# Kernel optimization log

Hardware: AMD Instinct MI355X
Metric: run time of the kernel (lower is better)

Reference implementation:

```python
import jax, jax.numpy as jnp
import numpy as np

N_P, N_D, N_S = 100000, 1000, 5000      # patients, drugs, diseases
C, H, L = 64, 4, 2                       # hidden, heads, layers
DH = C // H                              # head dim
IN_P, IN_D, IN_S = 64, 128, 64           # raw feature dims per node type
E_PD, E_DP, E_DS, E_PS = 300000, 300000, 100000, 100000
EPS = 1e-16


def setup_inputs() -> dict:
    key = jax.random.key(0)
    ks = jax.random.split(key, 20)

    def lin(k, fin, fout, prefix=()):
        return jax.random.normal(k, prefix + (fin, fout), jnp.float32) / np.sqrt(fin).astype(np.float32)

    def edges(k, e, n_src, n_dst):
        k1, k2 = jax.random.split(k)
        return jnp.stack([jax.random.randint(k1, (e,), 0, n_src),
                          jax.random.randint(k2, (e,), 0, n_dst)]).astype(jnp.int32)

    inp = {}
    inp['x_p'] = jax.random.normal(ks[0], (N_P, IN_P), jnp.float32)
    inp['x_d'] = jax.random.normal(ks[1], (N_D, IN_D), jnp.float32)
    inp['x_s'] = jax.random.normal(ks[2], (N_S, IN_S), jnp.float32)
    inp['Win_p'] = lin(ks[3], IN_P, C); inp['bin_p'] = jnp.zeros((C,), jnp.float32)
    inp['Win_d'] = lin(ks[4], IN_D, C); inp['bin_d'] = jnp.zeros((C,), jnp.float32)
    inp['Win_s'] = lin(ks[5], IN_S, C); inp['bin_s'] = jnp.zeros((C,), jnp.float32)
    inp['Wk'] = lin(ks[6], C, C, (L, 3)); inp['bk'] = jnp.zeros((L, 3, C), jnp.float32)
    inp['Wq'] = lin(ks[7], C, C, (L, 3)); inp['bq'] = jnp.zeros((L, 3, C), jnp.float32)
    inp['Wv'] = lin(ks[8], C, C, (L, 3)); inp['bv'] = jnp.zeros((L, 3, C), jnp.float32)
    inp['Wa'] = lin(ks[9], C, C, (L, 3)); inp['ba'] = jnp.zeros((L, 3, C), jnp.float32)
    inp['a_rel'] = jax.random.normal(ks[10], (L, 4, H, DH, DH), jnp.float32) / np.sqrt(DH).astype(np.float32)
    inp['m_rel'] = jax.random.normal(ks[11], (L, 4, H, DH, DH), jnp.float32) / np.sqrt(DH).astype(np.float32)
    inp['p_rel'] = jnp.ones((L, 4, H), jnp.float32)   # PyG inits rel prior to ones
    inp['skip'] = jnp.ones((L, 3), jnp.float32)       # PyG inits skip gate to ones
    inp['ei_pd'] = edges(ks[12], E_PD, N_P, N_D)  # patient -takes-> drug
    inp['ei_dp'] = edges(ks[13], E_DP, N_D, N_P)  # drug -taken_by-> patient
    inp['ei_ds'] = edges(ks[14], E_DS, N_D, N_S)  # drug -treats-> disease
    inp['ei_ps'] = edges(ks[15], E_PS, N_P, N_S)  # patient -has-> disease
    return inp


def _hgt(x_p, x_d, x_s, Win_p, bin_p, Win_d, bin_d, Win_s, bin_s,
         Wk, bk, Wq, bq, Wv, bv, Wa, ba, a_rel, m_rel, p_rel, skip,
         ei_pd, ei_dp, ei_ds, ei_ps):
    Ns = (N_P, N_D, N_S)
    # per-node-type input projection (lin_dict)
    xs = [x_p @ Win_p + bin_p, x_d @ Win_d + bin_d, x_s @ Win_s + bin_s]
    # (src_type, dst_type, edge_index) for each relation
    edge_defs = [(0, 1, ei_pd), (1, 0, ei_dp), (1, 2, ei_ds), (0, 2, ei_ps)]
    inv_sqrt_d = np.float32(1.0 / np.sqrt(DH))

    for l in range(L):  # HGTConv layers
        k_t = [(xs[t] @ Wk[l, t] + bk[l, t]).reshape(Ns[t], H, DH) for t in range(3)]
        q_t = [(xs[t] @ Wq[l, t] + bq[l, t]).reshape(Ns[t], H, DH) for t in range(3)]
        v_t = [(xs[t] @ Wv[l, t] + bv[l, t]).reshape(Ns[t], H, DH) for t in range(3)]
        out = [jnp.zeros((Ns[t], H, DH), xs[t].dtype) for t in range(3)]
        for r, (st, dt, ei) in enumerate(edge_defs):
            src, dst = ei[0], ei[1]
            # relation-specific head-wise transforms of K and V
            k_rel = jnp.einsum('nhd,hde->nhe', k_t[st], a_rel[l, r])
            v_rel = jnp.einsum('nhd,hde->nhe', v_t[st], m_rel[l, r])
            # attention logits per edge, per head: [E, H]
            alpha = (q_t[dt][dst] * k_rel[src]).sum(-1) * (p_rel[l, r] * inv_sqrt_d)
            # segment softmax over incoming edges of each dst node (per relation)
            mx = jax.ops.segment_max(alpha, dst, num_segments=Ns[dt])
            a = jnp.exp(alpha - jax.lax.stop_gradient(mx)[dst])
            den = jax.ops.segment_sum(a, dst, num_segments=Ns[dt])
            a = a / (den[dst] + EPS)
            # attention-weighted scatter-add of messages, grouped by 'sum'
            out[dt] = out[dt] + jax.ops.segment_sum(v_rel[src] * a[:, :, None], dst, num_segments=Ns[dt])
        new_xs = []
        for t in range(3):
            o = jax.nn.gelu(out[t].reshape(Ns[t], C), approximate=False) @ Wa[l, t] + ba[l, t]
            s = jax.nn.sigmoid(skip[l, t])  # learned skip gate (in == out channels)
            new_xs.append(s * o + (1.0 - s) * xs[t])
        xs = new_xs
    # concatenate node-type outputs along node axis: [N_P+N_D+N_S, C]
    return jnp.concatenate(xs, axis=0)


def reference(x_p, x_d, x_s, Win_p, bin_p, Win_d, bin_d, Win_s, bin_s,
              Wk, bk, Wq, bq, Wv, bv, Wa, ba, a_rel, m_rel, p_rel, skip,
              ei_pd, ei_dp, ei_ds, ei_ps):
    return _hgt(x_p, x_d, x_s, Win_p, bin_p, Win_d, bin_d, Win_s, bin_s,
                Wk, bk, Wq, bq, Wv, bv, Wa, ba, a_rel, m_rel, p_rel, skip,
                ei_pd, ei_dp, ei_ds, ei_ps)
```

## Files before the change

kernel.cpp:

```cpp
#include <hip/hip_runtime.h>
#include <cmath>

typedef unsigned short ush;
typedef __attribute__((ext_vector_type(8))) short short8;
typedef __attribute__((ext_vector_type(4))) float floatx4;

static constexpr int N_P = 100000, N_D = 1000, N_S = 5000, NT = N_P + N_D + N_S;
static constexpr int NC = 111000;
static constexpr int E_TOT = 800000;

static constexpr int NB0 = 128, NB2 = 64, NB3 = 64;
static constexpr int CH0 = (300000 + NB0 - 1) / NB0;
static constexpr int CH2 = (100000 + NB2 - 1) / NB2;
static constexpr int HB0_OFF = 0;
static constexpr int HB2_OFF = NB0 * 1000;
static constexpr int HB3_OFF = HB2_OFF + NB2 * 5000;
static constexpr int NCH0 = NB0 / 16, NCH2 = NB2 / 16;
static constexpr int CS0_OFF = 0;
static constexpr int CS2_OFF = NCH0 * 1000;
static constexpr int CS3_OFF = CS2_OFF + NCH2 * 5000;
static constexpr int NHIST = NB0 + NB2 + NB3;
static constexpr int NBLK_R1 = (300000 + 255) / 256;
static constexpr int NZB = (100000 + 255) / 256;

__device__ __forceinline__ float b2f(ush b) { return __uint_as_float(((unsigned)b) << 16); }
__device__ __forceinline__ ush f2b(float f) {
    unsigned u = __float_as_uint(f);
    return (ush)((u + 0x7FFFu + ((u >> 16) & 1u)) >> 16);
}

static constexpr size_t OFF_WINP = 0;
static constexpr size_t OFF_BINP = 4096;
static constexpr size_t OFF_WIND = 4160;
static constexpr size_t OFF_BIND = 12352;
static constexpr size_t OFF_WINS = 12416;
static constexpr size_t OFF_BINS = 16512;
static constexpr size_t OFF_WK = 16576;
static constexpr size_t OFF_BK = 41152;
static constexpr size_t OFF_WQ = 41536;
static constexpr size_t OFF_BQ = 66112;
static constexpr size_t OFF_WV = 66496;
static constexpr size_t OFF_BV = 91072;
static constexpr size_t OFF_WA = 91456;
static constexpr size_t OFF_BA = 116032;
static constexpr size_t OFF_AREL = 116416;
static constexpr size_t OFF_MREL = 124608;
static constexpr size_t OFF_PREL = 132800;
static constexpr size_t OFF_SKIP = 132832;
static constexpr size_t CW_TOTAL = 132838;
static constexpr int NCONVB = (int)((CW_TOTAL + 255) / 256);
static constexpr int NSCB = (NC + 1 + 255) / 256;

static constexpr size_t TWINP = 0;
static constexpr size_t TWIND = 4096;
static constexpr size_t TWINS = 12288;
static constexpr size_t TWQO = 16384;
static constexpr size_t TWAO = 40960;
static constexpr size_t TW_TOTAL = 65536;
static constexpr int NTWB = (int)(TW_TOTAL / 256);

struct ConvArgs {
    const void* src[18];
    long cum[19];
    int fl[18];
};

struct CsrB {
    const int* ei[3];
    const int* ei1;
};

__device__ __forceinline__ void hist_geom(int b, const CsrB& c, int& r, const int*& ei, int& E,
                                          int& ndst, int& e0, int& e1, int& hb) {
    if (b < NB0) {
        r = 0; ei = c.ei[0]; E = 300000; ndst = 1000;
        e0 = b * CH0; hb = HB0_OFF + b * 1000;
    } else if (b < NB0 + NB2) {
        r = 1; ei = c.ei[1]; E = 100000; ndst = 5000;
        e0 = (b - NB0) * CH2; hb = HB2_OFF + (b - NB0) * 5000;
    } else {
        r = 2; ei = c.ei[2]; E = 100000; ndst = 5000;
        e0 = (b - NB0 - NB2) * CH2; hb = HB3_OFF + (b - NB0 - NB2) * 5000;
    }
    e1 = min(E, e0 + ((r == 0) ? CH0 : CH2));
}

__device__ __forceinline__ bool cs_geom(int g, int& idx0, int& step) {
    if (g >= 48000) return false;
    if (g < 8000) {
        int c = g / 1000, d = g % 1000;
        idx0 = HB0_OFF + c * 16 * 1000 + d; step = 1000;
    } else if (g < 28000) {
        int gg = g - 8000, c = gg / 5000, d = gg % 5000;
        idx0 = HB2_OFF + c * 16 * 5000 + d; step = 5000;
    } else {
        int gg = g - 28000, c = gg / 5000, d = gg % 5000;
        idx0 = HB3_OFF + c * 16 * 5000 + d; step = 5000;
    }
    return true;
}

__global__ __launch_bounds__(256) void k1_kernel(ConvArgs a, ush* __restrict__ dst,
                                                 ush* __restrict__ tw,
                                                 int* __restrict__ cnt_r1, CsrB c,
                                                 int* __restrict__ HB) {
    const int b = blockIdx.x;
    if (b < NCONVB) {
        long g = (long)b * 256 + threadIdx.x;
        if (g >= (long)CW_TOTAL) return;
        int t = 0;
        while (g >= a.cum[t + 1]) t++;
        long i = g - a.cum[t];
        float v = a.fl[t] ? ((const float*)a.src[t])[i] : b2f(((const ush*)a.src[t])[i]);
        dst[g] = f2b(v);
    } else if (b < NCONVB + NZB) {
        int g = (b - NCONVB) * 256 + threadIdx.x;
        if (g < 100000) cnt_r1[g] = 0;
    } else if (b < NCONVB + NZB + NHIST) {
        __shared__ int h[5000];
        int r, E, ndst, e0, e1, hb;
        const int* ei;
        hist_geom(b - NCONVB - NZB, c, r, ei, E, ndst, e0, e1, hb);
        for (int d = threadIdx.x; d < ndst; d += 256) h[d] = 0;
        __syncthreads();
        for (int e = e0 + threadIdx.x; e < e1; e += 256) atomicAdd(&h[ei[E + e]], 1);
        __syncthreads();
        for (int d = threadIdx.x; d < ndst; d += 256) HB[hb + d] = h[d];
    } else {
        int g = (b - NCONVB - NZB - NHIST) * 256 + threadIdx.x;
        const void* src; int fl; long ibase; int e;
        if (g < 4096) { src = a.src[0]; fl = a.fl[0]; e = g; ibase = 0; }
        else if (g < 12288) { src = a.src[2]; fl = a.fl[2]; e = g - 4096; ibase = 0; }
        else if (g < 16384) { src = a.src[4]; fl = a.fl[4]; e = g - 12288; ibase = 0; }
        else if (g < 40960) { int ee = g - 16384; src = a.src[8]; fl = a.fl[8];
                              e = ee & 4095; ibase = (long)(ee >> 12) * 4096; }
        else { int ee = g - 40960; src = a.src[12]; fl = a.fl[12];
               e = ee & 4095; ibase = (long)(ee >> 12) * 4096; }
        int f = e >> 9, l = (e >> 3) & 63, j = e & 7;
        int s = f >> 2, cc = f & 3;
        long in = ibase + (long)(32 * s + ((l >> 4) << 3) + j) * 64 + 16 * cc + (l & 15);
        float v = fl ? ((const float*)src)[in] : b2f(((const ush*)src)[in]);
        tw[g] = f2b(v);
    }
}

template <int K>
__device__ __forceinline__ void stage_A(short* sA, const ush* __restrict__ X, int M, int row0) {
    for (int cid = threadIdx.x; cid < 64 * K / 8; cid += 256) {
        int r = cid / (K / 8), c0 = (cid % (K / 8)) * 8;
        int row = row0 + r;
        short8 v = {0, 0, 0, 0, 0, 0, 0, 0};
        if (row < M) v = *(const short8*)(const void*)(X + (size_t)row * K + c0);
        *(short8*)(&sA[r * (K + 8) + c0]) = v;
    }
}

template <int K>
__device__ __forceinline__ void stage_A_raw(short* sA, const void* __restrict__ X, int f,
                                            int M, int row0) {
    for (int cid = threadIdx.x; cid < 64 * K / 8; cid += 256) {
        int r = cid / (K / 8), c0 = (cid % (K / 8)) * 8;
        int row = row0 + r;
        short8 v = {0, 0, 0, 0, 0, 0, 0, 0};
        if (row < M) {
            if (f) {
                const floatx4* fp = (const floatx4*)((const float*)X + (size_t)row * K + c0);
                floatx4 f0 = fp[0], f1 = fp[1];
#pragma unroll
                for (int j = 0; j < 4; j++) v[j] = (short)f2b(f0[j]);
#pragma unroll
                for (int j = 0; j < 4; j++) v[4 + j] = (short)f2b(f1[j]);
            } else {
                v = *(const short8*)(const void*)((const ush*)X + (size_t)row * K + c0);
            }
        }
        *(short8*)(&sA[r * (K + 8) + c0]) = v;
    }
}

template <int K>
__device__ __forceinline__ void gemm_core64(const short* sA, short* sB,
                                            const ush* __restrict__ W, const ush* __restrict__ Bb,
                                            ush* __restrict__ Y, int M, int row0) {
    constexpr int NF = (K / 32) * 4;
    const int tid = threadIdx.x;
    for (int u = tid; u < NF * 64; u += 256)
        *(short8*)(&sB[u * 8]) = *(const short8*)(const void*)(W + (size_t)u * 8);
    __syncthreads();
    const int w = tid >> 6, l = tid & 63;
    floatx4 acc[4];
#pragma unroll
    for (int c = 0; c < 4; c++) {
        float bv = b2f(Bb[16 * c + (l & 15)]);
        acc[c] = (floatx4){bv, bv, bv, bv};
    }
#pragma unroll
    for (int s = 0; s < K / 32; s++) {
        short8 a = *(const short8*)(&sA[(16 * w + (l & 15)) * (K + 8) + 32 * s + ((l >> 4) << 3)]);
#pragma unroll
        for (int c = 0; c < 4; c++) {
            short8 b = *(const short8*)(&sB[(s * 4 + c) * 512 + l * 8]);
            acc[c] = __builtin_amdgcn_mfma_f32_16x16x32_bf16(a, b, acc[c], 0, 0, 0);
        }
    }
    __syncthreads();
#pragma unroll
    for (int c = 0; c < 4; c++)
#pragma unroll
        for (int r = 0; r < 4; r++)
            sB[(16 * w + ((l >> 4) << 2) + r) * 72 + 16 * c + (l & 15)] =
                (short)f2b(acc[c][r]);
    __syncthreads();
    for (int u = tid; u < 512; u += 256) {
        int r = u >> 3, c0 = (u & 7) * 8;
        int row = row0 + r;
        if (row < M)
            *(short8*)(Y + (size_t)row * 64 + c0) = *(const short8*)(&sB[r * 72 + c0]);
    }
}

template <int NG>
__device__ __forceinline__ void gemm_wide(const short* sA, short* sB,
                                          const ush* __restrict__ Wq, const ush* __restrict__ Bq,
                                          ush* __restrict__ Yq,
                                          const ush* __restrict__ WeA,
                                          ush* __restrict__ YAk, ush* __restrict__ YAv,
                                          const ush* __restrict__ WeB,
                                          ush* __restrict__ YBk, ush* __restrict__ YBv,
                                          int M, int row0) {
    constexpr int NF = 2 * NG;
    const int tid = threadIdx.x;
    for (int u = tid; u < NF * 64; u += 256) {
        int f = u >> 6, k = u & 63;
        int s = f / NG, c = f % NG;
        const ush* src;
        if (c < 4) src = Wq + (size_t)(s * 4 + c) * 512;
        else if (c < 12) src = WeA + (size_t)(s * 8 + (c - 4)) * 512;
        else src = WeB + (size_t)(s * 8 + (c - 12)) * 512;
        *(short8*)(&sB[f * 512 + k * 8]) = *(const short8*)(const void*)(src + k * 8);
    }
    __syncthreads();
    const int w = tid >> 6, l = tid & 63;
    floatx4 acc[NG];
#pragma unroll
    for (int c = 0; c < NG; c++) {
        float bv;
        if (c < 4) bv = b2f(Bq[16 * c + (l & 15)]);
        else if (c < 12) bv = b2f(WeA[8192 + 16 * (c - 4) + (l & 15)]);
        else bv = b2f(WeB[8192 + 16 * (c - 12) + (l & 15)]);
        acc[c] = (floatx4){bv, bv, bv, bv};
    }
#pragma unroll
    for (int s = 0; s < 2; s++) {
        short8 a = *(const short8*)(&sA[(16 * w + (l & 15)) * 72 + 32 * s + ((l >> 4) << 3)]);
#pragma unroll
        for (int c = 0; c < NG; c++) {
            short8 b = *(const short8*)(&sB[(s * NG + c) * 512 + l * 8]);
            acc[c] = __builtin_amdgcn_mfma_f32_16x16x32_bf16(a, b, acc[c], 0, 0, 0);
        }
    }
    ush* dst[5] = {Yq, YAk, YAv, YBk, YBv};
#pragma unroll
    for (int cg = 0; cg < NG / 4; cg++) {
        __syncthreads();
#pragma unroll
        for (int c2 = 0; c2 < 4; c2++)
#pragma unroll
            for (int r = 0; r < 4; r++)
                sB[(16 * w + ((l >> 4) << 2) + r) * 72 + 16 * c2 + (l & 15)] =
                    (short)f2b(acc[cg * 4 + c2][r]);
        __syncthreads();
        ush* Y = dst[cg];
        for (int u = tid; u < 512; u += 256) {
            int r = u >> 3, c0 = (u & 7) * 8;
            int row = row0 + r;
            if (row < M)
                *(short8*)(Y + (size_t)row * 64 + c0) = *(const short8*)(&sB[r * 72 + c0]);
        }
    }
}

struct K2Args {
    const void* raw[3];
    int f[3];
    const ush* W[3];
    const ush* Bb[3];
    ush* X;
    const int* HB;
    int* CS;
    int* cnt;
    const int* ei1;
};

__global__ __launch_bounds__(256) void k2_kernel(K2Args a) {
    extern __shared__ short smem[];
    const int b = blockIdx.x;
    if (b < 1658) {
        if (b < 1563) {
            short* sA = smem; short* sB = smem + 64 * 72;
            stage_A_raw<64>(sA, a.raw[0], a.f[0], N_P, b * 64);
            gemm_core64<64>(sA, sB, a.W[0], a.Bb[0], a.X, N_P, b * 64);
        } else if (b < 1579) {
            short* sA = smem; short* sB = smem + 64 * 136;
            stage_A_raw<128>(sA, a.raw[1], a.f[1], N_D, (b - 1563) * 64);
            gemm_core64<128>(sA, sB, a.W[1], a.Bb[1], a.X + (size_t)N_P * 64, N_D,
                             (b - 1563) * 64);
        } else {
            short* sA = smem; short* sB = smem + 64 * 72;
            stage_A_raw<64>(sA, a.raw[2], a.f[2], N_S, (b - 1579) * 64);
            gemm_core64<64>(sA, sB, a.W[2], a.Bb[2], a.X + (size_t)(N_P + N_D) * 64, N_S,
                            (b - 1579) * 64);
        }
    } else if (b < 1701) {
        int d = (b - 1658) * 256 + threadIdx.x;
        if (d >= 11000) return;
        int ld_, nch, base, step, cs0, csstep, roff;
        if (d < 1000) { ld_ = d; nch = NCH0; base = HB0_OFF + ld_; step = 1000;
                        cs0 = CS0_OFF + ld_; csstep = 1000; roff = 0; }
        else if (d < 6000) { ld_ = d - 1000; nch = NCH2; base = HB2_OFF + ld_; step = 5000;
                             cs0 = CS2_OFF + ld_; csstep = 5000; roff = 101000; }
        else { ld_ = d - 6000; nch = NCH2; base = HB3_OFF + ld_; step = 5000;
               cs0 = CS3_OFF + ld_; csstep = 5000; roff = 106000; }
        int run = 0;
        for (int cc = 0; cc < nch; cc++) {
            int s = 0;
#pragma unroll
            for (int bb = 0; bb < 16; bb++) s += a.HB[base + (cc * 16 + bb) * step];
            a.CS[cs0 + cc * csstep] = run;
            run += s;
        }
        a.cnt[roff + ld_] = run;
    } else {
        int g = (b - 1701) * 256 + threadIdx.x;
        if (g < 300000) atomicAdd(&a.cnt[1000 + a.ei1[300000 + g]], 1);
    }
}

__global__ __launch_bounds__(256) void k3_kernel(const int* __restrict__ cnt,
                                                 int* __restrict__ tmp,
                                                 int* __restrict__ part,
                                                 const ush* __restrict__ CW,
                                                 ush* __restrict__ weff) {
    const int b = blockIdx.x;
    if (b < 109) {
        __shared__ int ls[256];
        const int t = threadIdx.x;
        const int base = b * 1024 + t * 4;
        int v[4];
#pragma unroll
        for (int j = 0; j < 4; j++) v[j] = (base + j < NC) ? cnt[base + j] : 0;
        int tsum = v[0] + v[1] + v[2] + v[3];
        ls[t] = tsum;
        __syncthreads();
        for (int off = 1; off < 256; off <<= 1) {
            int y = (t >= off) ? ls[t - off] : 0;
            __syncthreads();
            ls[t] += y;
            __syncthreads();
        }
        int run = ls[t] - tsum;
#pragma unroll
        for (int j = 0; j < 4; j++) {
            if (base + j < NC) tmp[base + j] = run;
            run += v[j];
        }
        if (t == 255) part[b] = ls[255];
    } else {
        const int eb = b - 109;
        const int l = eb >> 2, r = eb & 3;
        const int st_of[4] = {0, 1, 1, 0};
        const int st = st_of[r];
        ush* out = weff + (size_t)eb * 8320;
        for (int idx = threadIdx.x; idx < 8320; idx += 256) {
            int k, n;
            if (idx < 8192) {
                int f = idx >> 9, ll = (idx >> 3) & 63, j = idx & 7;
                int s = f >> 3, c = f & 7;
                k = 32 * s + ((ll >> 4) << 3) + j;
                n = 16 * c + (ll & 15);
            } else { k = -1; n = idx - 8192; }
            int kv = n >= 64;
            int jj = n & 63, h = jj >> 4, e = jj & 15;
            const ush* W = CW + (kv ? OFF_WV : OFF_WK) + (size_t)(l * 3 + st) * 4096;
            const ush* B = CW + (kv ? OFF_BV : OFF_BK) + (size_t)(l * 3 + st) * 64;
            const ush* R = CW + (kv ? OFF_MREL : OFF_AREL) + (size_t)(l * 4 + r) * 1024;
            float acc = 0.f;
            if (k >= 0) {
#pragma unroll
                for (int d = 0; d < 16; d++)
                    acc += b2f(W[k * 64 + h * 16 + d]) * b2f(R[h * 256 + d * 16 + e]);
            } else {
#pragma unroll
                for (int d = 0; d < 16; d++)
                    acc += b2f(B[h * 16 + d]) * b2f(R[h * 256 + d * 16 + e]);
            }
            out[idx] = f2b(acc);
        }
    }
}

__global__ __launch_bounds__(256) void k4_kernel(const int* __restrict__ tmp,
                                                 const int* __restrict__ part,
                                                 int* __restrict__ rowptr,
                                                 int* __restrict__ HB,
                                                 const int* __restrict__ CS,
                                                 int* __restrict__ fillpos) {
    const int b = blockIdx.x;
    if (b < NSCB) {
        __shared__ int ls[256];
        const int t = threadIdx.x;
        ls[t] = (t < 109) ? part[t] : 0;
        __syncthreads();
        for (int off = 1; off < 256; off <<= 1) {
            int y = (t >= off) ? ls[t - off] : 0;
            __syncthreads();
            ls[t] += y;
            __syncthreads();
        }
        int i = b * 256 + t;
        if (i <= NC)
            rowptr[i] = (i == NC) ? ls[255] : tmp[i] + ((i >> 10) ? ls[(i >> 10) - 1] : 0);
    } else if (b < NSCB + 188) {
        int g = (b - NSCB) * 256 + threadIdx.x;
        int idx0, step;
        if (!cs_geom(g, idx0, step)) return;
        int run = CS[g];
#pragma unroll
        for (int bb = 0; bb < 16; bb++) {
            int t2 = HB[idx0 + bb * step];
            HB[idx0 + bb * step] = run;
            run += t2;
        }
    } else {
        int g = (b - NSCB - 188) * 256 + threadIdx.x;
        if (g < 100000) fillpos[g] = 0;
    }
}

struct QKVArgs {
    const ush* X;
    ush* Q;
    ush* KVk[4];
    ush* KVv[4];
    const ush* Wq[3];
    const ush* Bq[3];
    const ush* We[4];
};

__global__ __launch_bounds__(256) void qkv_kernel(QKVArgs a) {
    extern __shared__ short smem[];
    const int b = blockIdx.x;
    short* sA = smem;
    short* sB = smem + 64 * 72;
    if (b < 1563) {
        stage_A<64>(sA, a.X, N_P, b * 64);
        gemm_wide<20>(sA, sB, a.Wq[0], a.Bq[0], a.Q,
                      a.We[0], a.KVk[0], a.KVv[0],
                      a.We[3], a.KVk[3], a.KVv[3], N_P, b * 64);
    } else if (b < 1579) {
        int lb = b - 1563;
        stage_A<64>(sA, a.X + (size_t)N_P * 64, N_D, lb * 64);
        gemm_wide<20>(sA, sB, a.Wq[1], a.Bq[1], a.Q + (size_t)N_P * 64,
                      a.We[1], a.KVk[1], a.KVv[1],
                      a.We[2], a.KVk[2], a.KVv[2], N_D, lb * 64);
    } else {
        int lb = b - 1579;
        stage_A<64>(sA, a.X + (size_t)(N_P + N_D) * 64, N_S, lb * 64);
        gemm_wide<4>(sA, sB, a.Wq[2], a.Bq[2], a.Q + (size_t)(N_P + N_D) * 64,
                     nullptr, nullptr, nullptr, nullptr, nullptr, nullptr,
                     N_S, lb * 64);
    }
}

struct FillArgs {
    CsrB cb;
    const int* HB;
    const int* rowptr;
    int* fillpos;
    int* col;
};

__global__ __launch_bounds__(256) void fill_kernel(FillArgs a) {
    extern __shared__ short smem[];
    const int b = blockIdx.x;
    if (b < NHIST) {
        int* h = (int*)smem;
        int r, E, ndst, e0, e1, hb;
        const int* ei;
        hist_geom(b, a.cb, r, ei, E, ndst, e0, e1, hb);
        const int roff = (r == 0) ? 0 : (r == 1) ? 101000 : 106000;
        for (int d = threadIdx.x; d < ndst; d += 256) h[d] = a.rowptr[roff + d] + a.HB[hb + d];
        __syncthreads();
        for (int e = e0 + threadIdx.x; e < e1; e += 256) {
            int d = ei[E + e];
            int slot = atomicAdd(&h[d], 1);
            a.col[slot] = ei[e];
        }
    } else {
        int g = (b - NHIST) * 256 + threadIdx.x;
        if (g < 300000) {
            int gi = 1000 + a.cb.ei1[300000 + g];
            int slot = a.rowptr[gi] + atomicAdd(&a.fillpos[gi], 1);
            a.col[slot] = a.cb.ei1[g];
        }
    }
}

struct AggrArgs {
    const int* rowptr;
    const int* col;
    const ush* KVk[4];
    const ush* KVv[4];
    const ush* Q;
    const ush* prel;
    ush* OUT;
};

template <int LANES>
__device__ __forceinline__ void seg_attn(const AggrArgs& a, int rel, int g, int h, int lane,
                                         const float* qf, float* o) {
    const int s0 = a.rowptr[g], s1 = a.rowptr[g + 1];
    const ush* Kb = a.KVk[rel];
    const ush* Vb = a.KVv[rel];
    const float ps = b2f(a.prel[rel * 4 + h]) * 0.25f;
    float m = -1e30f, s = 0.f;
    float acc[16];
#pragma unroll
    for (int i = 0; i < 16; i++) acc[i] = 0.f;
    int j = s0 + lane;
    if (j < s1) {
        {
            int src = a.col[j];
            const ush* kp = Kb + (size_t)src * 64 + h * 16;
            const ush* vp = Vb + (size_t)src * 64 + h * 16;
            short8 k0 = *(const short8*)(const void*)kp;
            short8 k1 = *(const short8*)(const void*)(kp + 8);
            short8 v0 = *(const short8*)(const void*)vp;
            short8 v1 = *(const short8*)(const void*)(vp + 8);
            float dot = 0.f;
#pragma unroll
            for (int i = 0; i < 8; i++) dot += qf[i] * b2f((ush)k0[i]);
#pragma unroll
            for (int i = 0; i < 8; i++) dot += qf[8 + i] * b2f((ush)k1[i]);
            m = dot * ps;
            s = 1.f;
#pragma unroll
            for (int i = 0; i < 8; i++) acc[i] = b2f((ush)v0[i]);
#pragma unroll
            for (int i = 0; i < 8; i++) acc[8 + i] = b2f((ush)v1[i]);
        }
        for (j += LANES; j < s1; j += LANES) {
            int src = a.col[j];
            const ush* kp = Kb + (size_t)src * 64 + h * 16;
            const ush* vp = Vb + (size_t)src * 64 + h * 16;
            short8 k0 = *(const short8*)(const void*)kp;
            short8 k1 = *(const short8*)(const void*)(kp + 8);
            short8 v0 = *(const short8*)(const void*)vp;
            short8 v1 = *(const short8*)(const void*)(vp + 8);
            float dot = 0.f;
#pragma unroll
            for (int i = 0; i < 8; i++) dot += qf[i] * b2f((ush)k0[i]);
#pragma unroll
            for (int i = 0; i < 8; i++) dot += qf[8 + i] * b2f((ush)k1[i]);
            float e1 = __expf(dot * ps - m);
            s += e1;
#pragma unroll
            for (int i = 0; i < 8; i++) acc[i] += e1 * b2f((ush)v0[i]);
#pragma unroll
            for (int i = 0; i < 8; i++) acc[8 + i] += e1 * b2f((ush)v1[i]);
        }
    }
#pragma unroll
    for (int wd = LANES >> 1; wd >= 1; wd >>= 1) {
        float mo = __shfl_xor(m, wd);
        float so = __shfl_xor(s, wd);
        float nm = fmaxf(m, mo);
        float e0 = __expf(m - nm), e1 = __expf(mo - nm);
        s = s * e0 + so * e1;
#pragma unroll
        for (int i = 0; i < 16; i++) {
            float ao = __shfl_xor(acc[i], wd);
            acc[i] = acc[i] * e0 + ao * e1;
        }
        m = nm;
    }
    float inv = 1.f / (s + 1e-16f);
#pragma unroll
    for (int i = 0; i < 16; i++) o[i] += acc[i] * inv;
}

template <int LANES>
__device__ __forceinline__ void job_run(const AggrArgs& a, int wid, int nd, int rel, int roff,
                                        size_t xoff, int rel2, int roff2) {
    const int lane = wid % LANES;
    const int grp = wid / LANES;
    const int d = grp >> 2, h = grp & 3;
    if (d >= nd) return;
    const ush* qp = a.Q + xoff + (size_t)d * 64 + h * 16;
    short8 q0 = *(const short8*)(const void*)qp;
    short8 q1 = *(const short8*)(const void*)(qp + 8);
    float qf[16];
#pragma unroll
    for (int i = 0; i < 8; i++) { qf[i] = b2f((ush)q0[i]); qf[8 + i] = b2f((ush)q1[i]); }
    float o[16];
#pragma unroll
    for (int i = 0; i < 16; i++) o[i] = 0.f;
    seg_attn<LANES>(a, rel, roff + d, h, lane, qf, o);
    if (rel2 >= 0) seg_attn<LANES>(a, rel2, roff2 + d, h, lane, qf, o);
    if (lane == 0) {
        ush* op = a.OUT + xoff + (size_t)d * 64 + h * 16;
        short8 w0, w1;
#pragma unroll
        for (int i = 0; i < 8; i++) {
            float va = o[i];
            w0[i] = (short)f2b(0.5f * va * (1.0f + erff(va * 0.70710678118654752f)));
            float vb = o[8 + i];
            w1[i] = (short)f2b(0.5f * vb * (1.0f + erff(vb * 0.70710678118654752f)));
        }
        *(short8*)(op) = w0;
        *(short8*)(op + 8) = w1;
    }
}

__global__ __launch_bounds__(256) void aggr_kernel(AggrArgs a) {
    const int b = blockIdx.x, t = threadIdx.x;
    if (b < 250) {
        job_run<16>(a, b * 256 + t, N_D, 0, 0, (size_t)N_P * 64, -1, 0);
    } else if (b < 563) {
        job_run<4>(a, (b - 250) * 256 + t, N_S, 2, 101000, (size_t)(N_P + N_D) * 64, 3, 106000);
    } else {
        job_run<2>(a, (b - 563) * 256 + t, N_P, 1, 1000, 0, -1, 0);
    }
}

struct EpiArgs {
    const ush* O;
    ush* X;
    const ush* W[3];
    const ush* Bb[3];
    const ush* skipv;
    void* fout;
    int foutf;
    int last;
};

__global__ __launch_bounds__(256) void epi_kernel(EpiArgs a) {
    const int b = blockIdx.x;
    int t, lb, M;
    size_t noff;
    if (b < 1563) { t = 0; lb = b; M = N_P; noff = 0; }
    else if (b < 1579) { t = 1; lb = b - 1563; M = N_D; noff = (size_t)N_P; }
    else { t = 2; lb = b - 1579; M = N_S; noff = (size_t)(N_P + N_D); }
    const ush* O = a.O + noff * 64;
    ush* X = a.X + noff * 64;
    const ush* WF = a.W[t];
    __shared__ short sA[64 * 72];
    __shared__ short sB[8 * 512];
    const int tid = threadIdx.x;
    const int row0 = lb * 64;
    for (int cid = tid; cid < 512; cid += 256) {
        int r = cid >> 3, c0 = (cid & 7) * 8;
        int row = row0 + r;
        short8 sv = {0, 0, 0, 0, 0, 0, 0, 0};
        if (row < M) sv = *(const short8*)(const void*)(O + (size_t)row * 64 + c0);
        *(short8*)(&sA[r * 72 + c0]) = sv;
    }
    for (int u = tid; u < 512; u += 256)
        *(short8*)(&sB[u * 8]) = *(const short8*)(const void*)(WF + (size_t)u * 8);
    __syncthreads();
    const float sg = 1.f / (1.f + expf(-b2f(a.skipv[t])));
    const int w = tid >> 6, l = tid & 63;
    floatx4 acc[4];
#pragma unroll
    for (int c = 0; c < 4; c++) {
        float bv = b2f(a.Bb[t][16 * c + (l & 15)]);
        acc[c] = (floatx4){bv, bv, bv, bv};
    }
#pragma unroll
    for (int s = 0; s < 2; s++) {
        short8 av = *(const short8*)(&sA[(16 * w + (l & 15)) * 72 + 32 * s + ((l >> 4) << 3)]);
#pragma unroll
        for (int c = 0; c < 4; c++) {
            short8 bv = *(const short8*)(&sB[(s * 4 + c) * 512 + l * 8]);
            acc[c] = __builtin_amdgcn_mfma_f32_16x16x32_bf16(av, bv, acc[c], 0, 0, 0);
        }
    }
    float* sOf = (float*)sA;
#pragma unroll
    for (int ch = 0; ch < 2; ch++) {
        __syncthreads();
        if ((w >> 1) == ch) {
#pragma unroll
            for (int c = 0; c < 4; c++)
#pragma unroll
                for (int r = 0; r < 4; r++)
                    sOf[(16 * (w & 1) + ((l >> 4) << 2) + r) * 68 + 16 * c + (l & 15)] =
                        acc[c][r];
        }
        __syncthreads();
        {
            int r = tid >> 3, c0 = (tid & 7) * 8;
            int row = row0 + ch * 32 + r;
            if (row < M) {
                floatx4 f0 = *(const floatx4*)(&sOf[r * 68 + c0]);
                floatx4 f1 = *(const floatx4*)(&sOf[r * 68 + c0 + 4]);
                short8 xv = *(const short8*)(const void*)(X + (size_t)row * 64 + c0);
                float vo[8];
#pragma unroll
                for (int j = 0; j < 4; j++) vo[j] = sg * f0[j] + (1.f - sg) * b2f((ush)xv[j]);
#pragma unroll
                for (int j = 0; j < 4; j++)
                    vo[4 + j] = sg * f1[j] + (1.f - sg) * b2f((ush)xv[4 + j]);
                if (!a.last) {
                    short8 ov;
#pragma unroll
                    for (int j = 0; j < 8; j++) ov[j] = (short)f2b(vo[j]);
                    *(short8*)(X + (size_t)row * 64 + c0) = ov;
                } else {
                    size_t goff = (noff + row) * 64 + c0;
                    if (a.foutf) {
                        floatx4 o0, o1;
#pragma unroll
                        for (int j = 0; j < 4; j++) { o0[j] = vo[j]; o1[j] = vo[4 + j]; }
                        *(floatx4*)((float*)a.fout + goff) = o0;
                        *(floatx4*)((float*)a.fout + goff + 4) = o1;
                    } else {
                        short8 ov;
#pragma unroll
                        for (int j = 0; j < 8; j++) ov[j] = (short)f2b(vo[j]);
                        *(short8*)((ush*)a.fout + goff) = ov;
                    }
                }
            }
        }
    }
}

extern "C" void kernel_launch(void* const* d_in, const int* in_sizes, int n_in,
                              void* d_out, int out_size, void* d_ws, size_t ws_size,
                              hipStream_t stream) {
    char* w = (char*)d_ws;
    w += 64;
    ush* CW = (ush*)w;      w += ((CW_TOTAL * 2 + 63) / 64) * 64;
    ush* WEFFB = (ush*)w;   w += ((size_t)8 * 8320 * 2 + 63) / 64 * 64;
    ush* TW = (ush*)w;      w += (size_t)TW_TOTAL * 2;
    ush* X = (ush*)w;       w += (size_t)NT * 64 * 2;
    ush* Q = (ush*)w;       w += (size_t)NT * 64 * 2;
    ush* KV0 = (ush*)w;     w += (size_t)N_P * 128 * 2;
    ush* KV1 = (ush*)w;     w += (size_t)N_D * 128 * 2;
    ush* KV2 = (ush*)w;     w += (size_t)N_D * 128 * 2;
    ush* KV3 = (ush*)w;     w += (size_t)N_P * 128 * 2;
    ush* OUT = (ush*)w;     w += (size_t)NT * 64 * 4;
    int* CNT = (int*)w;     w += (size_t)NC * 4;
    int* TMP = (int*)w;     w += (size_t)NC * 4;
    int* PART = (int*)w;    w += 512;
    int* ROWPTR = (int*)w;  w += (size_t)(NC + 1) * 4;
    int* COL = (int*)w;     w += (size_t)E_TOT * 4;
    int* HB = (int*)OUT;
    int* CS = (int*)OUT + 800000;

    static const long sz[18] = {4096, 64, 8192, 64, 4096, 64, 24576, 384, 24576, 384,
                                24576, 384, 24576, 384, 8192, 8192, 32, 6};
    ConvArgs ca;
    long cum = 0;
    for (int t = 0; t < 18; t++) {
        ca.src[t] = d_in[3 + t];
        ca.cum[t] = cum;
        ca.fl[t] = (in_sizes[3 + t] != (int)(sz[t] * 2)) ? 1 : 0;
        cum += sz[t];
    }
    ca.cum[18] = cum;

    CsrB cb;
    cb.ei[0] = (const int*)d_in[21];
    cb.ei[1] = (const int*)d_in[23];
    cb.ei[2] = (const int*)d_in[24];
    cb.ei1 = (const int*)d_in[22];

    k1_kernel<<<NCONVB + NZB + NHIST + NTWB, 256, 0, stream>>>(ca, CW, TW, CNT + 1000, cb, HB);

    K2Args k2;
    k2.raw[0] = d_in[0]; k2.f[0] = (in_sizes[0] != N_P * 64 * 2) ? 1 : 0;
    k2.raw[1] = d_in[1]; k2.f[1] = (in_sizes[1] != N_D * 128 * 2) ? 1 : 0;
    k2.raw[2] = d_in[2]; k2.f[2] = (in_sizes[2] != N_S * 64 * 2) ? 1 : 0;
    k2.W[0] = TW + TWINP; k2.Bb[0] = CW + OFF_BINP;
    k2.W[1] = TW + TWIND; k2.Bb[1] = CW + OFF_BIND;
    k2.W[2] = TW + TWINS; k2.Bb[2] = CW + OFF_BINS;
    k2.X = X;
    k2.HB = HB; k2.CS = CS; k2.cnt = CNT; k2.ei1 = cb.ei1;
    k2_kernel<<<1701 + NBLK_R1, 256, 33792, stream>>>(k2);

    k3_kernel<<<109 + 8, 256, 0, stream>>>(CNT, TMP, PART, CW, WEFFB);

    k4_kernel<<<NSCB + 188 + NZB, 256, 0, stream>>>(TMP, PART, ROWPTR, HB, CS, CNT + 1000);

    ush* KVr[4] = {KV0, KV1, KV2, KV3};
    const size_t nsr[4] = {(size_t)N_P, (size_t)N_D, (size_t)N_D, (size_t)N_P};
    const int foutf = (out_size != NT * 64 * 2) ? 1 : 0;

    for (int l = 0; l < 2; l++) {
        QKVArgs qk;
        qk.X = X;
        qk.Q = Q;
        for (int r = 0; r < 4; r++) {
            qk.KVk[r] = KVr[r];
            qk.KVv[r] = KVr[r] + nsr[r] * 64;
            qk.We[r] = WEFFB + (size_t)(l * 4 + r) * 8320;
        }
        for (int t = 0; t < 3; t++) {
            qk.Wq[t] = TW + TWQO + (size_t)(l * 3 + t) * 4096;
            qk.Bq[t] = CW + OFF_BQ + (l * 3 + t) * 64;
        }
        qkv_kernel<<<1658, 256, 50176, stream>>>(qk);

        if (l == 0) {
            FillArgs fa;
            fa.cb = cb;
            fa.HB = HB;
            fa.rowptr = ROWPTR;
            fa.fillpos = CNT;
            fa.col = COL;
            fill_kernel<<<NHIST + NBLK_R1, 256, 20000, stream>>>(fa);
        }

        AggrArgs aa;
        aa.rowptr = ROWPTR;
        aa.col = COL;
        for (int r = 0; r < 4; r++) {
            aa.KVk[r] = KVr[r];
            aa.KVv[r] = KVr[r] + nsr[r] * 64;
        }
        aa.Q = Q;
        aa.prel = CW + OFF_PREL + l * 16;
        aa.OUT = OUT;
        aggr_kernel<<<3688, 256, 0, stream>>>(aa);

        EpiArgs ea;
        ea.O = OUT;
        ea.X = X;
        for (int t = 0; t < 3; t++) {
            ea.W[t] = TW + TWAO + (size_t)(l * 3 + t) * 4096;
            ea.Bb[t] = CW + OFF_BA + (l * 3 + t) * 64;
        }
        ea.skipv = CW + OFF_SKIP + l * 3;
        ea.fout = d_out;
        ea.foutf = foutf;
        ea.last = (l == 1) ? 1 : 0;
        epi_kernel<<<1658, 256, 0, stream>>>(ea);
    }
}
```

Baseline: 386.0 us.

## Process QKV GEMM in 64-column panels and widen aggregation lanes for hubs

The fused Q/K/V projection now loads weights and runs MFMAs one 64-column output panel at a time, reusing a small shared buffer, instead of staging all 20 column groups at once. This cuts dynamic shared memory from about 50 KB to about 17 KB and drops the 20-accumulator register array, aiming at higher occupancy, in exchange for more barriers and repeated weight staging. Separately, the aggregation kernel gives more lanes per destination node for the high-degree drug and disease segments, launching more blocks to spread their long edge lists.

```diff
diff --git a/kernel.cpp b/kernel.cpp
--- a/kernel.cpp
+++ b/kernel.cpp
@@ -219,63 +219,62 @@
     }
 }
 
-template <int NG>
-__device__ __forceinline__ void gemm_wide(const short* sA, short* sB,
-                                          const ush* __restrict__ Wq, const ush* __restrict__ Bq,
-                                          ush* __restrict__ Yq,
-                                          const ush* __restrict__ WeA,
-                                          ush* __restrict__ YAk, ush* __restrict__ YAv,
-                                          const ush* __restrict__ WeB,
-                                          ush* __restrict__ YBk, ush* __restrict__ YBv,
-                                          int M, int row0) {
-    constexpr int NF = 2 * NG;
+template <int NP>
+__device__ __forceinline__ void gemm_panels(short* sA, short* sB,
+                                            const ush* __restrict__ Wq,
+                                            const ush* __restrict__ Bq, ush* __restrict__ Yq,
+                                            const ush* __restrict__ WeA,
+                                            ush* __restrict__ YAk, ush* __restrict__ YAv,
+                                            const ush* __restrict__ WeB,
+                                            ush* __restrict__ YBk, ush* __restrict__ YBv,
+                                            int M, int row0) {
     const int tid = threadIdx.x;
-    for (int u = tid; u < NF * 64; u += 256) {
-        int f = u >> 6, k = u & 63;
-        int s = f / NG, c = f % NG;
-        const ush* src;
-        if (c < 4) src = Wq + (size_t)(s * 4 + c) * 512;
-        else if (c < 12) src = WeA + (size_t)(s * 8 + (c - 4)) * 512;
-        else src = WeB + (size_t)(s * 8 + (c - 12)) * 512;
-        *(short8*)(&sB[f * 512 + k * 8]) = *(const short8*)(const void*)(src + k * 8);
-    }
+    const int w = tid >> 6, l = tid & 63;
     __syncthreads();
-    const int w = tid >> 6, l = tid & 63;
-    floatx4 acc[NG];
-#pragma unroll
-    for (int c = 0; c < NG; c++) {
-        float bv;
-        if (c < 4) bv = b2f(Bq[16 * c + (l & 15)]);
-        else if (c < 12) bv = b2f(WeA[8192 + 16 * (c - 4) + (l & 15)]);
-        else bv = b2f(WeB[8192 + 16 * (c - 12) + (l & 15)]);
-        acc[c] = (floatx4){bv, bv, bv, bv};
-    }
-#pragma unroll
-    for (int s = 0; s < 2; s++) {
-        short8 a = *(const short8*)(&sA[(16 * w + (l & 15)) * 72 + 32 * s + ((l >> 4) << 3)]);
-#pragma unroll
-        for (int c = 0; c < NG; c++) {
-            short8 b = *(const short8*)(&sB[(s * NG + c) * 512 + l * 8]);
-            acc[c] = __builtin_amdgcn_mfma_f32_16x16x32_bf16(a, b, acc[c], 0, 0, 0);
-        }
-    }
+    short8 a0 = *(const short8*)(&sA[(16 * w + (l & 15)) * 72 + ((l >> 4) << 3)]);
+    short8 a1 = *(const short8*)(&sA[(16 * w + (l & 15)) * 72 + 32 + ((l >> 4) << 3)]);
     ush* dst[5] = {Yq, YAk, YAv, YBk, YBv};
 #pragma unroll
-    for (int cg = 0; cg < NG / 4; cg++) {
-        __syncthreads();
-#pragma unroll
-        for (int c2 = 0; c2 < 4; c2++)
+    for (int p = 0; p < NP; p++) {
+        __syncthreads();
+        const ush* base = (p == 0) ? Wq : ((p <= 2) ? WeA : WeB);
+        const int nw = (p == 0) ? 4 : 8;
+        const int moff = (p == 0 || p == 1 || p == 3) ? 0 : 4;
+        for (int u = tid; u < 512; u += 256) {
+            int f = u >> 6, k = u & 63;
+            int s = f >> 2, c = f & 3;
+            const ush* src = base + (size_t)(s * nw + moff + c) * 512;
+            *(short8*)(&sB[f * 512 + k * 8]) = *(const short8*)(const void*)(src + k * 8);
+        }
+        __syncthreads();
+        const ush* bias = (p == 0) ? Bq : ((p <= 2) ? WeA + 8192 : WeB + 8192);
+        const int boff = (p == 0 || p == 1 || p == 3) ? 0 : 64;
+        floatx4 acc[4];
+#pragma unroll
+        for (int c = 0; c < 4; c++) {
+            float bv = b2f(bias[boff + 16 * c + (l & 15)]);
+            acc[c] = (floatx4){bv, bv, bv, bv};
+        }
+#pragma unroll
+        for (int c = 0; c < 4; c++) {
+            short8 b0 = *(const short8*)(&sB[c * 512 + l * 8]);
+            acc[c] = __builtin_amdgcn_mfma_f32_16x16x32_bf16(a0, b0, acc[c], 0, 0, 0);
+            short8 b1 = *(const short8*)(&sB[(4 + c) * 512 + l * 8]);
+            acc[c] = __builtin_amdgcn_mfma_f32_16x16x32_bf16(a1, b1, acc[c], 0, 0, 0);
+        }
+#pragma unroll
+        for (int c = 0; c < 4; c++)
 #pragma unroll
             for (int r = 0; r < 4; r++)
-                sB[(16 * w + ((l >> 4) << 2) + r) * 72 + 16 * c2 + (l & 15)] =
-                    (short)f2b(acc[cg * 4 + c2][r]);
-        __syncthreads();
-        ush* Y = dst[cg];
+                sA[(16 * w + ((l >> 4) << 2) + r) * 72 + 16 * c + (l & 15)] =
+                    (short)f2b(acc[c][r]);
+        __syncthreads();
+        ush* Y = dst[p];
         for (int u = tid; u < 512; u += 256) {
             int r = u >> 3, c0 = (u & 7) * 8;
             int row = row0 + r;
             if (row < M)
-                *(short8*)(Y + (size_t)row * 64 + c0) = *(const short8*)(&sB[r * 72 + c0]);
+                *(short8*)(Y + (size_t)row * 64 + c0) = *(const short8*)(&sA[r * 72 + c0]);
         }
     }
 }
@@ -454,21 +453,21 @@
     short* sB = smem + 64 * 72;
     if (b < 1563) {
         stage_A<64>(sA, a.X, N_P, b * 64);
-        gemm_wide<20>(sA, sB, a.Wq[0], a.Bq[0], a.Q,
-                      a.We[0], a.KVk[0], a.KVv[0],
-                      a.We[3], a.KVk[3], a.KVv[3], N_P, b * 64);
+        gemm_panels<5>(sA, sB, a.Wq[0], a.Bq[0], a.Q,
+                       a.We[0], a.KVk[0], a.KVv[0],
+                       a.We[3], a.KVk[3], a.KVv[3], N_P, b * 64);
     } else if (b < 1579) {
         int lb = b - 1563;
         stage_A<64>(sA, a.X + (size_t)N_P * 64, N_D, lb * 64);
-        gemm_wide<20>(sA, sB, a.Wq[1], a.Bq[1], a.Q + (size_t)N_P * 64,
-                      a.We[1], a.KVk[1], a.KVv[1],
-                      a.We[2], a.KVk[2], a.KVv[2], N_D, lb * 64);
+        gemm_panels<5>(sA, sB, a.Wq[1], a.Bq[1], a.Q + (size_t)N_P * 64,
+                       a.We[1], a.KVk[1], a.KVv[1],
+                       a.We[2], a.KVk[2], a.KVv[2], N_D, lb * 64);
     } else {
         int lb = b - 1579;
         stage_A<64>(sA, a.X + (size_t)(N_P + N_D) * 64, N_S, lb * 64);
-        gemm_wide<4>(sA, sB, a.Wq[2], a.Bq[2], a.Q + (size_t)(N_P + N_D) * 64,
-                     nullptr, nullptr, nullptr, nullptr, nullptr, nullptr,
-                     N_S, lb * 64);
+        gemm_panels<1>(sA, sB, a.Wq[2], a.Bq[2], a.Q + (size_t)(N_P + N_D) * 64,
+                       nullptr, nullptr, nullptr, nullptr, nullptr, nullptr,
+                       N_S, lb * 64);
     }
 }
 
@@ -624,12 +623,12 @@
 
 __global__ __launch_bounds__(256) void aggr_kernel(AggrArgs a) {
     const int b = blockIdx.x, t = threadIdx.x;
-    if (b < 250) {
-        job_run<16>(a, b * 256 + t, N_D, 0, 0, (size_t)N_P * 64, -1, 0);
-    } else if (b < 563) {
-        job_run<4>(a, (b - 250) * 256 + t, N_S, 2, 101000, (size_t)(N_P + N_D) * 64, 3, 106000);
+    if (b < 1000) {
+        job_run<64>(a, b * 256 + t, N_D, 0, 0, (size_t)N_P * 64, -1, 0);
+    } else if (b < 2250) {
+        job_run<16>(a, (b - 1000) * 256 + t, N_S, 2, 101000, (size_t)(N_P + N_D) * 64, 3, 106000);
     } else {
-        job_run<2>(a, (b - 563) * 256 + t, N_P, 1, 1000, 0, -1, 0);
+        job_run<2>(a, (b - 2250) * 256 + t, N_P, 1, 1000, 0, -1, 0);
     }
 }
 
@@ -811,7 +810,7 @@
             qk.Wq[t] = TW + TWQO + (size_t)(l * 3 + t) * 4096;
             qk.Bq[t] = CW + OFF_BQ + (l * 3 + t) * 64;
         }
-        qkv_kernel<<<1658, 256, 50176, stream>>>(qk);
+        qkv_kernel<<<1658, 256, 17408, stream>>>(qk);
 
         if (l == 0) {
             FillArgs fa;
@@ -833,7 +832,7 @@
         aa.Q = Q;
         aa.prel = CW + OFF_PREL + l * 16;
         aa.OUT = OUT;
-        aggr_kernel<<<3688, 256, 0, stream>>>(aa);
+        aggr_kernel<<<5375, 256, 0, stream>>>(aa);
 
         EpiArgs ea;
         ea.O = OUT;
```

Result: faster. 358.9 us (-7.0%).
